# Performance work log

Measured on AMD Instinct MI355X. Metric: run time of the kernel, lower is better.

The kernel has to match this reference:

```python
import jax, jax.numpy as jnp
import numpy as np

B, NQ, NKV, D = 2, 2048, 4096, 1024
H, DH = 16, 64            # qk_channels = v_channels = 1024 -> 16 heads x 64
HID = 2 * int(4.0 * D)    # GEGLU produces 8192 -> split into 2x4096
EPS = 1e-6


def layernorm(x, scale, bias):
    mu = jnp.mean(x, axis=-1, keepdims=True)
    var = jnp.mean(jnp.square(x - mu), axis=-1, keepdims=True)
    return (x - mu) * jax.lax.rsqrt(var + EPS) * scale + bias


def setup_inputs() -> dict:
    key = jax.random.key(0)
    ks = jax.random.split(key, 12)
    s = 0.02
    return {
        "inputs_q": jax.random.normal(ks[0], (B, NQ, D), jnp.float32),
        "inputs_kv": jax.random.normal(ks[1], (B, NKV, D), jnp.float32),
        "ln_q_scale": jnp.ones((D,), jnp.float32),
        "ln_q_bias": jnp.zeros((D,), jnp.float32),
        "ln_kv_scale": jnp.ones((D,), jnp.float32),
        "ln_kv_bias": jnp.zeros((D,), jnp.float32),
        "Wq": s * jax.random.normal(ks[2], (D, H, DH), jnp.float32),
        "bq": jnp.zeros((H, DH), jnp.float32),
        "Wk": s * jax.random.normal(ks[3], (D, H, DH), jnp.float32),
        "bk": jnp.zeros((H, DH), jnp.float32),
        "Wv": s * jax.random.normal(ks[4], (D, H, DH), jnp.float32),
        "bv": jnp.zeros((H, DH), jnp.float32),
        "Wo": s * jax.random.normal(ks[5], (H, DH, D), jnp.float32),
        "bo": jnp.zeros((D,), jnp.float32),
        "ln2_scale": jnp.ones((D,), jnp.float32),
        "ln2_bias": jnp.zeros((D,), jnp.float32),
        "W1": s * jax.random.normal(ks[6], (D, HID), jnp.float32),
        "b1": jnp.zeros((HID,), jnp.float32),
        "W2": s * jax.random.normal(ks[7], (HID // 2, D), jnp.float32),
        "b2": jnp.zeros((D,), jnp.float32),
    }


def reference(inputs_q, inputs_kv, ln_q_scale, ln_q_bias, ln_kv_scale, ln_kv_bias,
              Wq, bq, Wk, bk, Wv, bv, Wo, bo, ln2_scale, ln2_bias, W1, b1, W2, b2):
    ln_q = layernorm(inputs_q, ln_q_scale, ln_q_bias)
    ln_kv = layernorm(inputs_kv, ln_kv_scale, ln_kv_bias)
    # multi-head projections: DenseGeneral to (H, DH)
    q = jnp.einsum('bqd,dhe->bqhe', ln_q, Wq) + bq
    k = jnp.einsum('bkd,dhe->bkhe', ln_kv, Wk) + bk
    v = jnp.einsum('bkd,dhe->bkhe', ln_kv, Wv) + bv
    # scaled dot-product attention (full score matrix, as in source)
    attn = jnp.einsum('bqhd,bkhd->bhqk', q, k) / np.sqrt(DH).astype(np.float32)
    attn = jax.nn.softmax(attn, axis=-1)
    o = jnp.einsum('bhqk,bkhd->bqhd', attn, v)
    # output projection contracting (H, DH)
    x = jnp.einsum('bqhd,hdo->bqo', o, Wo) + bo
    x = x + inputs_q  # query residual
    # GEGLU MLP
    h = layernorm(x, ln2_scale, ln2_bias)
    h = jnp.dot(h, W1) + b1
    a, g = jnp.split(h, 2, axis=-1)
    h = a * jax.nn.gelu(g)  # approximate (tanh) gelu, flax default
    y = jnp.dot(h, W2) + b2
    return x + y
```

## Files before the change

### kernel.cpp

```cpp
#include <hip/hip_runtime.h>

typedef unsigned short u16;
typedef unsigned int u32;
typedef float f32x4 __attribute__((ext_vector_type(4)));
typedef float f32x16 __attribute__((ext_vector_type(16)));
typedef __bf16 bf16x8 __attribute__((ext_vector_type(8)));
typedef short s16x8 __attribute__((ext_vector_type(8)));
typedef short s16x4 __attribute__((ext_vector_type(4)));
typedef u32 u32x4 __attribute__((ext_vector_type(4)));

#define MFMA16(a, b, c) __builtin_amdgcn_mfma_f32_16x16x32_bf16((a), (b), (c), 0, 0, 0)
#define MFMA32(a, b, c) __builtin_amdgcn_mfma_f32_32x32x16_bf16((a), (b), (c), 0, 0, 0)

typedef const __attribute__((address_space(1))) void* gas1_t;
typedef __attribute__((address_space(3))) void* las3_t;
#define GLDS16(g, l) __builtin_amdgcn_global_load_lds((gas1_t)(g), (las3_t)(l), 16, 0, 0)

static __device__ __forceinline__ u16 f2bf(float f) {
  u32 u = __builtin_bit_cast(u32, f);
  u += 0x7FFFu + ((u >> 16) & 1u);
  return (u16)(u >> 16);
}
static __device__ __forceinline__ float bf2f(u16 h) {
  return __builtin_bit_cast(float, (u32)h << 16);
}
static __device__ __forceinline__ u32 cvtpk(float lo, float hi) {
  u32 r;
  asm("v_cvt_pk_bf16_f32 %0, %1, %2" : "=v"(r) : "v"(lo), "v"(hi));
  return r;
}
static __device__ __forceinline__ float gelu_t(float g) {
  float u = 0.7978845608f * (g + 0.044715f * g * g * g);
  float e = __expf(2.0f * u);
  float t = 1.0f - 2.0f / (e + 1.0f);
  return 0.5f * g * (1.0f + t);
}

__global__ __launch_bounds__(256) void transp_cvt(const float* __restrict__ in,
                                                  u16* __restrict__ out, int K, int N,
                                                  float scale) {
  __shared__ u16 t[64][72];
  int k0 = blockIdx.x * 64, n0 = blockIdx.y * 64;
#pragma unroll
  for (int i = 0; i < 16; ++i) {
    int idx = threadIdx.x + i * 256;
    int r = idx >> 6, c = idx & 63;
    t[r][c] = f2bf(in[(size_t)(k0 + r) * N + n0 + c] * scale);
  }
  __syncthreads();
#pragma unroll
  for (int i = 0; i < 16; ++i) {
    int idx = threadIdx.x + i * 256;
    int r = idx >> 6, c = idx & 63;
    out[(size_t)(n0 + r) * K + k0 + c] = t[c][r];
  }
}

__global__ __launch_bounds__(256) void geglu_transp(const float* __restrict__ in,
                                                    u16* __restrict__ out) {
  __shared__ u16 t[64][72];
  int k0 = blockIdx.x * 64, n0 = blockIdx.y * 64;
#pragma unroll
  for (int i = 0; i < 16; ++i) {
    int idx = threadIdx.x + i * 256;
    int r = idx >> 6, c = idx & 63;
    int np = n0 + c;
    int orig = ((np >> 5) << 4) + (np & 15) + (((np >> 4) & 1) << 12);
    t[r][c] = f2bf(in[(size_t)(k0 + r) * 8192 + orig]);
  }
  __syncthreads();
#pragma unroll
  for (int i = 0; i < 16; ++i) {
    int idx = threadIdx.x + i * 256;
    int r = idx >> 6, c = idx & 63;
    out[(size_t)(n0 + r) * 1024 + k0 + c] = t[c][r];
  }
}

__global__ __launch_bounds__(256) void ln_bf16(const float* __restrict__ x,
                                               const float* __restrict__ sc,
                                               const float* __restrict__ bi,
                                               u16* __restrict__ out) {
  int row = blockIdx.x;
  int tid = threadIdx.x;
  float4 v = ((const float4*)(x + (size_t)row * 1024))[tid];
  float s = v.x + v.y + v.z + v.w;
  float s2 = v.x * v.x + v.y * v.y + v.z * v.z + v.w * v.w;
  for (int m = 1; m < 64; m <<= 1) {
    s += __shfl_xor(s, m);
    s2 += __shfl_xor(s2, m);
  }
  __shared__ float rs[4], rs2[4];
  int wave = tid >> 6, lane = tid & 63;
  if (lane == 0) { rs[wave] = s; rs2[wave] = s2; }
  __syncthreads();
  s = rs[0] + rs[1] + rs[2] + rs[3];
  s2 = rs2[0] + rs2[1] + rs2[2] + rs2[3];
  float mu = s * (1.0f / 1024.0f);
  float var = s2 * (1.0f / 1024.0f) - mu * mu;
  float inv = rsqrtf(var + 1e-6f);
  float4 scv = ((const float4*)sc)[tid];
  float4 biv = ((const float4*)bi)[tid];
  s16x4 o;
  o[0] = (short)f2bf((v.x - mu) * inv * scv.x + biv.x);
  o[1] = (short)f2bf((v.y - mu) * inv * scv.y + biv.y);
  o[2] = (short)f2bf((v.z - mu) * inv * scv.z + biv.z);
  o[3] = (short)f2bf((v.w - mu) * inv * scv.w + biv.w);
  *(s16x4*)(out + (size_t)row * 1024 + tid * 4) = o;
}

template <int MODE>
__global__ __launch_bounds__(256) void gemm_nt(const u16* __restrict__ A,
                                               const u16* __restrict__ Bt,
                                               const float* __restrict__ bias,
                                               const float* __restrict__ resid,
                                               void* __restrict__ Cout,
                                               int M, int N, int K, float bias_scale) {
  __shared__ u16 As[128 * 64];
  __shared__ u16 Bs[128 * 64];
  const int nbx = gridDim.x;
  const int nwg = nbx * gridDim.y;
  const int wg0 = blockIdx.y * nbx + blockIdx.x;
  const int wg = (nwg & 7) ? wg0 : (wg0 & 7) * (nwg >> 3) + (wg0 >> 3);
  const int m0 = (wg % nbx) * 128, n0 = (wg / nbx) * 128;
  const int tid = threadIdx.x;
  const int lane = tid & 63, wave = tid >> 6;
  const int wm = (wave >> 1) * 64, wn = (wave & 1) * 64;
  const int lr = lane & 15, hi4 = lane >> 4;
  f32x4 acc[4][4] = {};
  for (int k0 = 0; k0 < K; k0 += 64) {
#pragma unroll
    for (int i = 0; i < 4; ++i) {
      int s = i * 256 + tid;
      int r = s >> 3, slot = s & 7;
      int gslot = slot ^ (r & 7);
      int ldst = (i * 256 + wave * 64) * 8;
      GLDS16(A + (size_t)(m0 + r) * K + k0 + gslot * 8, &As[ldst]);
      GLDS16(Bt + (size_t)(n0 + r) * K + k0 + gslot * 8, &Bs[ldst]);
    }
    __syncthreads();
#pragma unroll
    for (int ks = 0; ks < 2; ++ks) {
      const int sl = ((ks * 4 + hi4) ^ (lr & 7)) * 8;
      bf16x8 af[4], bfr[4];
#pragma unroll
      for (int t = 0; t < 4; ++t) {
        af[t] = __builtin_bit_cast(bf16x8, *(const s16x8*)&As[(wm + t * 16 + lr) * 64 + sl]);
        bfr[t] = __builtin_bit_cast(bf16x8, *(const s16x8*)&Bs[(wn + t * 16 + lr) * 64 + sl]);
      }
#pragma unroll
      for (int mt = 0; mt < 4; ++mt)
#pragma unroll
        for (int nt = 0; nt < 4; ++nt)
          acc[mt][nt] = MFMA16(af[mt], bfr[nt], acc[mt][nt]);
    }
    __syncthreads();
  }
  if constexpr (MODE == 3) {
#pragma unroll
    for (int mt = 0; mt < 4; ++mt) {
      const int mbase = m0 + wm + mt * 16 + hi4 * 4;
#pragma unroll
      for (int p = 0; p < 2; ++p) {
        const int oc = (((n0 + wn + p * 32) >> 5) << 4) + lr;
        const float ba = bias[oc];
        const float bg = bias[oc + 4096];
#pragma unroll
        for (int r = 0; r < 4; ++r) {
          const int m = mbase + r;
          float a = acc[mt][2 * p][r] + ba;
          float g = acc[mt][2 * p + 1][r] + bg;
          ((u16*)Cout)[(size_t)m * 4096 + oc] = f2bf(a * gelu_t(g));
        }
      }
    }
  } else {
#pragma unroll
    for (int mt = 0; mt < 4; ++mt) {
#pragma unroll
      for (int nt = 0; nt < 4; ++nt) {
        const int ncol = n0 + wn + nt * 16 + lr;
        const float bv = bias[ncol] * bias_scale;
        const int mbase = m0 + wm + mt * 16 + hi4 * 4;
#pragma unroll
        for (int r = 0; r < 4; ++r) {
          const int m = mbase + r;
          const float val = acc[mt][nt][r] + bv;
          if constexpr (MODE == 0) {
            ((u16*)Cout)[(size_t)m * N + ncol] = f2bf(val);
          } else if constexpr (MODE == 1) {
            size_t vidx = ((size_t)((m >> 12) * 1024 + ncol) << 12) | (size_t)(m & 4095);
            ((u16*)Cout)[vidx] = f2bf(val);
          } else {
            ((float*)Cout)[(size_t)m * N + ncol] = val + resid[(size_t)m * N + ncol];
          }
        }
      }
    }
  }
}

__global__ __launch_bounds__(256, 2) void flash_attn(const u16* __restrict__ Qg,
                                                     const u16* __restrict__ Kg,
                                                     const u16* __restrict__ Vt,
                                                     u16* __restrict__ Og) {
  __shared__ u16 Ks[2][64 * 64];
  __shared__ u16 Vs[2][64 * 64];
  const int id = blockIdx.x;
  const int bh = (id & 7) * 4 + ((id >> 3) & 3);
  const int qb = id >> 5;
  const int b = bh >> 4, h = bh & 15;
  const int q0 = qb * 128;
  const int tid = threadIdx.x;
  const int lane = tid & 63, wave = tid >> 6;
  const int lq = lane & 31, hi = lane >> 5;
  const u16* Kbase = Kg + (size_t)(b * 4096) * 1024 + h * 64;
  const u16* Vbase = Vt + (size_t)((b * 16 + h) * 64) * 4096;
  bf16x8 qf[4];
  const size_t qrow = (size_t)(b * 2048 + q0 + wave * 32 + lq);
#pragma unroll
  for (int dc = 0; dc < 4; ++dc)
    qf[dc] = __builtin_bit_cast(bf16x8, *(const s16x8*)&Qg[qrow * 1024 + h * 64 + dc * 16 + hi * 8]);

  f32x16 oacc0 = {}, oacc1 = {};
  float lrun = 0.0f;

  auto stage = [&](int buf, int tile) {
    const int kv0 = tile * 64;
#pragma unroll
    for (int i = 0; i < 2; ++i) {
      int s = i * 256 + tid;
      int r = s >> 3;
      int inb = ((s & 7) * 16) ^ ((r & 7) << 4);
      GLDS16(Kbase + (size_t)(kv0 + r) * 1024 + (inb >> 1), &Ks[buf][(i * 256 + wave * 64) * 8]);
    }
#pragma unroll
    for (int i = 0; i < 2; ++i) {
      int s = i * 256 + tid;
      int r = s >> 3;
      int inb = ((s & 7) * 16) ^ ((r & 7) << 4);
      GLDS16(Vbase + (size_t)r * 4096 + kv0 + (inb >> 1), &Vs[buf][(i * 256 + wave * 64) * 8]);
    }
  };

  stage(0, 0);
  __syncthreads();
  int cur = 0;
  for (int t = 0; t < 64; ++t) {
    if (t < 63) stage(cur ^ 1, t + 1);
    f32x16 sA = {}, sB = {};
    __builtin_amdgcn_s_setprio(1);
#pragma unroll
    for (int dc = 0; dc < 4; ++dc) {
      int row = lq;
      int inb = (dc * 32 + hi * 16) ^ ((row & 7) << 4);
      bf16x8 kf = __builtin_bit_cast(bf16x8, *(const s16x8*)&Ks[cur][row * 64 + (inb >> 1)]);
      sA = MFMA32(kf, qf[dc], sA);
    }
#pragma unroll
    for (int dc = 0; dc < 4; ++dc) {
      int row = 32 + lq;
      int inb = (dc * 32 + hi * 16) ^ ((row & 7) << 4);
      bf16x8 kf = __builtin_bit_cast(bf16x8, *(const s16x8*)&Ks[cur][row * 64 + (inb >> 1)]);
      sB = MFMA32(kf, qf[dc], sB);
    }
    __builtin_amdgcn_s_setprio(0);
#pragma unroll
    for (int i = 0; i < 16; ++i) sA[i] = __builtin_amdgcn_exp2f(sA[i]);
#pragma unroll
    for (int i = 0; i < 16; ++i) sB[i] = __builtin_amdgcn_exp2f(sB[i]);
    float a0 = (sA[0] + sA[1]) + (sA[2] + sA[3]);
    float a1 = (sA[4] + sA[5]) + (sA[6] + sA[7]);
    float a2 = (sA[8] + sA[9]) + (sA[10] + sA[11]);
    float a3 = (sA[12] + sA[13]) + (sA[14] + sA[15]);
    float b0 = (sB[0] + sB[1]) + (sB[2] + sB[3]);
    float b1s = (sB[4] + sB[5]) + (sB[6] + sB[7]);
    float b2s = (sB[8] + sB[9]) + (sB[10] + sB[11]);
    float b3 = (sB[12] + sB[13]) + (sB[14] + sB[15]);
    float ts = ((a0 + a1) + (a2 + a3)) + ((b0 + b1s) + (b2s + b3));
    ts += __shfl_xor(ts, 32);
    lrun += ts;
    u32 wa[8], wb[8];
#pragma unroll
    for (int i = 0; i < 8; ++i) wa[i] = cvtpk(sA[2 * i], sA[2 * i + 1]);
#pragma unroll
    for (int i = 0; i < 8; ++i) wb[i] = cvtpk(sB[2 * i], sB[2 * i + 1]);
    u32 a0w = wa[0], c0 = wa[2];
    asm("v_permlane32_swap_b32 %0, %1" : "+v"(a0w), "+v"(c0));
    u32 a1w = wa[1], c1 = wa[3];
    asm("v_permlane32_swap_b32 %0, %1" : "+v"(a1w), "+v"(c1));
    u32 a2w = wa[4], c2 = wa[6];
    asm("v_permlane32_swap_b32 %0, %1" : "+v"(a2w), "+v"(c2));
    u32 a3w = wa[5], c3 = wa[7];
    asm("v_permlane32_swap_b32 %0, %1" : "+v"(a3w), "+v"(c3));
    u32 e0 = wb[0], g0 = wb[2];
    asm("v_permlane32_swap_b32 %0, %1" : "+v"(e0), "+v"(g0));
    u32 e1 = wb[1], g1 = wb[3];
    asm("v_permlane32_swap_b32 %0, %1" : "+v"(e1), "+v"(g1));
    u32 e2 = wb[4], g2 = wb[6];
    asm("v_permlane32_swap_b32 %0, %1" : "+v"(e2), "+v"(g2));
    u32 e3 = wb[5], g3 = wb[7];
    asm("v_permlane32_swap_b32 %0, %1" : "+v"(e3), "+v"(g3));
    u32x4 t00 = {a0w, a1w, c0, c1};
    u32x4 t01 = {a2w, a3w, c2, c3};
    u32x4 t10 = {e0, e1, g0, g1};
    u32x4 t11 = {e2, e3, g2, g3};
    bf16x8 p00 = __builtin_bit_cast(bf16x8, t00);
    bf16x8 p01 = __builtin_bit_cast(bf16x8, t01);
    bf16x8 p10 = __builtin_bit_cast(bf16x8, t10);
    bf16x8 p11 = __builtin_bit_cast(bf16x8, t11);
    __builtin_amdgcn_s_setprio(1);
#pragma unroll
    for (int st = 0; st < 2; ++st) {
      bf16x8 pc0 = st ? p10 : p00;
      bf16x8 pc1 = st ? p11 : p01;
#pragma unroll
      for (int c = 0; c < 2; ++c) {
        bf16x8 pf = c ? pc1 : pc0;
        {
          int row = lq;
          int inb = (st * 64 + c * 32 + hi * 16) ^ ((row & 7) << 4);
          bf16x8 vf = __builtin_bit_cast(bf16x8, *(const s16x8*)&Vs[cur][row * 64 + (inb >> 1)]);
          oacc0 = MFMA32(vf, pf, oacc0);
        }
        {
          int row = 32 + lq;
          int inb = (st * 64 + c * 32 + hi * 16) ^ ((row & 7) << 4);
          bf16x8 vf = __builtin_bit_cast(bf16x8, *(const s16x8*)&Vs[cur][row * 64 + (inb >> 1)]);
          oacc1 = MFMA32(vf, pf, oacc1);
        }
      }
    }
    __builtin_amdgcn_s_setprio(0);
    __syncthreads();
    cur ^= 1;
  }
  float rinv = 1.0f / lrun;
  u16* obase = Og + qrow * 1024 + h * 64;
#pragma unroll
  for (int rp = 0; rp < 8; ++rp) {
    int r0 = rp * 2;
    int d0 = (r0 & 3) + 8 * (r0 >> 2) + 4 * hi;
    *(u32*)&obase[d0] = cvtpk(oacc0[r0] * rinv, oacc0[r0 + 1] * rinv);
    *(u32*)&obase[32 + d0] = cvtpk(oacc1[r0] * rinv, oacc1[r0 + 1] * rinv);
  }
}

extern "C" void kernel_launch(void* const* d_in, const int* in_sizes, int n_in,
                              void* d_out, int out_size, void* d_ws, size_t ws_size,
                              hipStream_t stream) {
  (void)in_sizes; (void)n_in; (void)out_size; (void)ws_size;
  const float* inputs_q = (const float*)d_in[0];
  const float* inputs_kv = (const float*)d_in[1];
  const float* ln_q_scale = (const float*)d_in[2];
  const float* ln_q_bias = (const float*)d_in[3];
  const float* ln_kv_scale = (const float*)d_in[4];
  const float* ln_kv_bias = (const float*)d_in[5];
  const float* Wq = (const float*)d_in[6];
  const float* bq = (const float*)d_in[7];
  const float* Wk = (const float*)d_in[8];
  const float* bk = (const float*)d_in[9];
  const float* Wv = (const float*)d_in[10];
  const float* bv = (const float*)d_in[11];
  const float* Wo = (const float*)d_in[12];
  const float* bo = (const float*)d_in[13];
  const float* ln2_scale = (const float*)d_in[14];
  const float* ln2_bias = (const float*)d_in[15];
  const float* W1 = (const float*)d_in[16];
  const float* b1 = (const float*)d_in[17];
  const float* W2 = (const float*)d_in[18];
  const float* b2 = (const float*)d_in[19];
  float* out = (float*)d_out;
  char* ws = (char*)d_ws;
  const size_t MB = 1ull << 20;
  u16* lnq = (u16*)(ws + 0);
  u16* lnkv = (u16*)(ws + 8 * MB);
  u16* Qb = (u16*)(ws + 24 * MB);
  u16* Kb = (u16*)(ws + 32 * MB);
  u16* Vtb = (u16*)(ws + 48 * MB);
  u16* Ob = (u16*)(ws + 64 * MB);
  float* xbuf = (float*)(ws + 72 * MB);
  u16* ln2b = (u16*)(ws + 88 * MB);
  u16* gg = (u16*)(ws + 96 * MB);
  u16* wqt = (u16*)(ws + 128 * MB);
  u16* wkt = (u16*)(ws + 130 * MB);
  u16* wvt = (u16*)(ws + 132 * MB);
  u16* wot = (u16*)(ws + 134 * MB);
  u16* w1i = (u16*)(ws + 136 * MB);
  u16* w2t = (u16*)(ws + 152 * MB);

  const float QSC = 0.125f * 1.44269504088896f;
  dim3 blk(256);
  transp_cvt<<<dim3(16, 16), blk, 0, stream>>>(Wq, wqt, 1024, 1024, QSC);
  transp_cvt<<<dim3(16, 16), blk, 0, stream>>>(Wk, wkt, 1024, 1024, 1.0f);
  transp_cvt<<<dim3(16, 16), blk, 0, stream>>>(Wv, wvt, 1024, 1024, 1.0f);
  transp_cvt<<<dim3(16, 16), blk, 0, stream>>>(Wo, wot, 1024, 1024, 1.0f);
  geglu_transp<<<dim3(16, 128), blk, 0, stream>>>(W1, w1i);
  transp_cvt<<<dim3(64, 16), blk, 0, stream>>>(W2, w2t, 4096, 1024, 1.0f);
  ln_bf16<<<4096, blk, 0, stream>>>(inputs_q, ln_q_scale, ln_q_bias, lnq);
  ln_bf16<<<8192, blk, 0, stream>>>(inputs_kv, ln_kv_scale, ln_kv_bias, lnkv);
  gemm_nt<0><<<dim3(32, 8), blk, 0, stream>>>(lnq, wqt, bq, nullptr, Qb, 4096, 1024, 1024, QSC);
  gemm_nt<0><<<dim3(64, 8), blk, 0, stream>>>(lnkv, wkt, bk, nullptr, Kb, 8192, 1024, 1024, 1.0f);
  gemm_nt<1><<<dim3(64, 8), blk, 0, stream>>>(lnkv, wvt, bv, nullptr, Vtb, 8192, 1024, 1024, 1.0f);
  flash_attn<<<dim3(512), blk, 0, stream>>>(Qb, Kb, Vtb, Ob);
  gemm_nt<2><<<dim3(32, 8), blk, 0, stream>>>(Ob, wot, bo, inputs_q, xbuf, 4096, 1024, 1024, 1.0f);
  ln_bf16<<<4096, blk, 0, stream>>>(xbuf, ln2_scale, ln2_bias, ln2b);
  gemm_nt<3><<<dim3(32, 64), blk, 0, stream>>>(ln2b, w1i, b1, nullptr, gg, 4096, 8192, 1024, 1.0f);
  gemm_nt<2><<<dim3(32, 8), blk, 0, stream>>>(gg, w2t, b2, xbuf, out, 4096, 1024, 4096, 1.0f);
}
```

Measured before the change: 410.5 us.

## Add 256x256 tiled GEMM kernel for fused K/V projection and GEGLU up-projection

Introduces a new 512-thread GEMM kernel with 256x256 output tiles, double-buffered LDS filled by direct global-to-LDS loads, explicit barriers/waitcnts, and MFMA priority hints. K and V projections are merged into one GEMM over a concatenated weight matrix, with the epilogue routing columns to the K buffer or the transposed V buffer. The GEGLU up-projection also moves to this kernel. The aim is more data reuse per tile and fewer launches, at the cost of higher register/LDS pressure and fewer blocks per GEMM.

New measurement: 409.5 us. Within noise of the previous version (-0.3%).

```diff
diff --git a/kernel.cpp b/kernel.cpp
--- a/kernel.cpp
+++ b/kernel.cpp
@@ -156,44 +156,167 @@
     }
     __syncthreads();
   }
-  if constexpr (MODE == 3) {
-#pragma unroll
-    for (int mt = 0; mt < 4; ++mt) {
+#pragma unroll
+  for (int mt = 0; mt < 4; ++mt) {
+#pragma unroll
+    for (int nt = 0; nt < 4; ++nt) {
+      const int ncol = n0 + wn + nt * 16 + lr;
+      const float bv = bias[ncol] * bias_scale;
       const int mbase = m0 + wm + mt * 16 + hi4 * 4;
 #pragma unroll
+      for (int r = 0; r < 4; ++r) {
+        const int m = mbase + r;
+        const float val = acc[mt][nt][r] + bv;
+        if constexpr (MODE == 0) {
+          ((u16*)Cout)[(size_t)m * N + ncol] = f2bf(val);
+        } else {
+          ((float*)Cout)[(size_t)m * N + ncol] = val + resid[(size_t)m * N + ncol];
+        }
+      }
+    }
+  }
+}
+
+template <int MODE>
+__global__ __launch_bounds__(512, 2) void gemm256(const u16* __restrict__ A,
+                                                  const u16* __restrict__ Bt,
+                                                  const float* __restrict__ bias,
+                                                  const float* __restrict__ bias2,
+                                                  u16* __restrict__ Cout,
+                                                  u16* __restrict__ Vout,
+                                                  int M, int N, int K, int nmajor) {
+  __shared__ __align__(16) u16 sA[2][2][256 * 32];
+  __shared__ __align__(16) u16 sB[2][2][256 * 32];
+  const int nbx = M >> 8, nby = N >> 8;
+  const int nblk = nbx * nby;
+  const int cpx = nblk >> 3;
+  const int wg0 = blockIdx.x;
+  const int wg = (wg0 & 7) * cpx + (wg0 >> 3);
+  int mi, ni;
+  if (nmajor) { ni = wg % nby; mi = wg / nby; } else { mi = wg % nbx; ni = wg / nbx; }
+  const int m0 = mi << 8, n0 = ni << 8;
+  const int tid = threadIdx.x;
+  const int lane = tid & 63, wave = tid >> 6;
+  const int wr = wave >> 2, wc = wave & 3;
+  const int lr = lane & 15, hi4 = lane >> 4;
+  const int rdoct = (hi4 ^ ((lr >> 1) & 3)) * 8;
+  const int NT = K >> 6;
+
+  auto stageA = [&](int t, int kh) {
+#pragma unroll
+    for (int i = 0; i < 2; ++i) {
+      int idx = i * 512 + tid;
+      int r = idx >> 2, go = (idx & 3) ^ ((r >> 1) & 3);
+      GLDS16(A + (size_t)(m0 + r) * K + t * 64 + kh * 32 + go * 8,
+             &sA[t & 1][kh][(i * 512 + wave * 64) * 8]);
+    }
+  };
+  auto stageB = [&](int t, int kh) {
+#pragma unroll
+    for (int i = 0; i < 2; ++i) {
+      int idx = i * 512 + tid;
+      int r = idx >> 2, go = (idx & 3) ^ ((r >> 1) & 3);
+      GLDS16(Bt + (size_t)(n0 + r) * K + t * 64 + kh * 32 + go * 8,
+             &sB[t & 1][kh][(i * 512 + wave * 64) * 8]);
+    }
+  };
+
+  f32x4 acc[8][4] = {};
+  bf16x8 af[4], bf[4];
+
+  stageA(0, 0); stageB(0, 0); stageA(0, 1); stageB(0, 1);
+  asm volatile("s_waitcnt vmcnt(4)" ::: "memory");
+  __builtin_amdgcn_s_barrier();
+  __builtin_amdgcn_sched_barrier(0);
+
+  for (int t = 0; t < NT; ++t) {
+    const int buf = t & 1;
+    const bool pre = (t + 1 < NT);
+#pragma unroll
+    for (int kh = 0; kh < 2; ++kh) {
+#pragma unroll
+      for (int nt = 0; nt < 4; ++nt)
+        bf[nt] = __builtin_bit_cast(bf16x8,
+            *(const s16x8*)&sB[buf][kh][(wc * 64 + nt * 16 + lr) * 32 + rdoct]);
+#pragma unroll
+      for (int mf = 0; mf < 4; ++mf)
+        af[mf] = __builtin_bit_cast(bf16x8,
+            *(const s16x8*)&sA[buf][kh][(wr * 128 + mf * 16 + lr) * 32 + rdoct]);
+      if (pre) stageA(t + 1, kh);
+      __builtin_amdgcn_s_barrier();
+      asm volatile("s_waitcnt lgkmcnt(0)" ::: "memory");
+      __builtin_amdgcn_sched_barrier(0);
+      __builtin_amdgcn_s_setprio(1);
+#pragma unroll
+      for (int mf = 0; mf < 4; ++mf)
+#pragma unroll
+        for (int nt = 0; nt < 4; ++nt)
+          acc[mf][nt] = MFMA16(af[mf], bf[nt], acc[mf][nt]);
+      __builtin_amdgcn_s_setprio(0);
+      __builtin_amdgcn_s_barrier();
+      __builtin_amdgcn_sched_barrier(0);
+#pragma unroll
+      for (int mf = 0; mf < 4; ++mf)
+        af[mf] = __builtin_bit_cast(bf16x8,
+            *(const s16x8*)&sA[buf][kh][(wr * 128 + (4 + mf) * 16 + lr) * 32 + rdoct]);
+      if (pre) stageB(t + 1, kh);
+      __builtin_amdgcn_s_barrier();
+      asm volatile("s_waitcnt lgkmcnt(0)" ::: "memory");
+      __builtin_amdgcn_sched_barrier(0);
+      __builtin_amdgcn_s_setprio(1);
+#pragma unroll
+      for (int mf = 0; mf < 4; ++mf)
+#pragma unroll
+        for (int nt = 0; nt < 4; ++nt)
+          acc[4 + mf][nt] = MFMA16(af[mf], bf[nt], acc[4 + mf][nt]);
+      __builtin_amdgcn_s_setprio(0);
+      if (pre)
+        asm volatile("s_waitcnt vmcnt(4)" ::: "memory");
+      else
+        asm volatile("s_waitcnt vmcnt(0)" ::: "memory");
+      __builtin_amdgcn_s_barrier();
+      __builtin_amdgcn_sched_barrier(0);
+    }
+  }
+
+  if constexpr (MODE == 0) {
+#pragma unroll
+    for (int mf = 0; mf < 8; ++mf) {
+#pragma unroll
+      for (int nt = 0; nt < 4; ++nt) {
+        const int ncol = n0 + wc * 64 + nt * 16 + lr;
+        const int mbase = m0 + wr * 128 + mf * 16 + hi4 * 4;
+        const bool isk = ncol < 1024;
+        const int vc = isk ? ncol : ncol - 1024;
+        const float bv = isk ? bias[ncol] : bias2[vc];
+#pragma unroll
+        for (int r = 0; r < 4; ++r) {
+          const int m = mbase + r;
+          const float val = acc[mf][nt][r] + bv;
+          if (isk) {
+            Cout[(size_t)m * 1024 + ncol] = f2bf(val);
+          } else {
+            size_t vidx = ((size_t)((m >> 12) * 1024 + vc) << 12) | (size_t)(m & 4095);
+            Vout[vidx] = f2bf(val);
+          }
+        }
+      }
+    }
+  } else {
+#pragma unroll
+    for (int mf = 0; mf < 8; ++mf) {
+      const int mbase = m0 + wr * 128 + mf * 16 + hi4 * 4;
+#pragma unroll
       for (int p = 0; p < 2; ++p) {
-        const int oc = (((n0 + wn + p * 32) >> 5) << 4) + lr;
+        const int oc = (((n0 + wc * 64 + p * 32) >> 5) << 4) + lr;
         const float ba = bias[oc];
         const float bg = bias[oc + 4096];
 #pragma unroll
         for (int r = 0; r < 4; ++r) {
           const int m = mbase + r;
-          float a = acc[mt][2 * p][r] + ba;
-          float g = acc[mt][2 * p + 1][r] + bg;
-          ((u16*)Cout)[(size_t)m * 4096 + oc] = f2bf(a * gelu_t(g));
-        }
-      }
-    }
-  } else {
-#pragma unroll
-    for (int mt = 0; mt < 4; ++mt) {
-#pragma unroll
-      for (int nt = 0; nt < 4; ++nt) {
-        const int ncol = n0 + wn + nt * 16 + lr;
-        const float bv = bias[ncol] * bias_scale;
-        const int mbase = m0 + wm + mt * 16 + hi4 * 4;
-#pragma unroll
-        for (int r = 0; r < 4; ++r) {
-          const int m = mbase + r;
-          const float val = acc[mt][nt][r] + bv;
-          if constexpr (MODE == 0) {
-            ((u16*)Cout)[(size_t)m * N + ncol] = f2bf(val);
-          } else if constexpr (MODE == 1) {
-            size_t vidx = ((size_t)((m >> 12) * 1024 + ncol) << 12) | (size_t)(m & 4095);
-            ((u16*)Cout)[vidx] = f2bf(val);
-          } else {
-            ((float*)Cout)[(size_t)m * N + ncol] = val + resid[(size_t)m * N + ncol];
-          }
+          float a = acc[mf][2 * p][r] + ba;
+          float g = acc[mf][2 * p + 1][r] + bg;
+          Cout[(size_t)m * 4096 + oc] = f2bf(a * gelu_t(g));
         }
       }
     }
@@ -383,8 +506,7 @@
   u16* ln2b = (u16*)(ws + 88 * MB);
   u16* gg = (u16*)(ws + 96 * MB);
   u16* wqt = (u16*)(ws + 128 * MB);
-  u16* wkt = (u16*)(ws + 130 * MB);
-  u16* wvt = (u16*)(ws + 132 * MB);
+  u16* wkvt = (u16*)(ws + 130 * MB);
   u16* wot = (u16*)(ws + 134 * MB);
   u16* w1i = (u16*)(ws + 136 * MB);
   u16* w2t = (u16*)(ws + 152 * MB);
@@ -392,19 +514,18 @@
   const float QSC = 0.125f * 1.44269504088896f;
   dim3 blk(256);
   transp_cvt<<<dim3(16, 16), blk, 0, stream>>>(Wq, wqt, 1024, 1024, QSC);
-  transp_cvt<<<dim3(16, 16), blk, 0, stream>>>(Wk, wkt, 1024, 1024, 1.0f);
-  transp_cvt<<<dim3(16, 16), blk, 0, stream>>>(Wv, wvt, 1024, 1024, 1.0f);
+  transp_cvt<<<dim3(16, 16), blk, 0, stream>>>(Wk, wkvt, 1024, 1024, 1.0f);
+  transp_cvt<<<dim3(16, 16), blk, 0, stream>>>(Wv, wkvt + 1024 * 1024, 1024, 1024, 1.0f);
   transp_cvt<<<dim3(16, 16), blk, 0, stream>>>(Wo, wot, 1024, 1024, 1.0f);
   geglu_transp<<<dim3(16, 128), blk, 0, stream>>>(W1, w1i);
   transp_cvt<<<dim3(64, 16), blk, 0, stream>>>(W2, w2t, 4096, 1024, 1.0f);
   ln_bf16<<<4096, blk, 0, stream>>>(inputs_q, ln_q_scale, ln_q_bias, lnq);
   ln_bf16<<<8192, blk, 0, stream>>>(inputs_kv, ln_kv_scale, ln_kv_bias, lnkv);
   gemm_nt<0><<<dim3(32, 8), blk, 0, stream>>>(lnq, wqt, bq, nullptr, Qb, 4096, 1024, 1024, QSC);
-  gemm_nt<0><<<dim3(64, 8), blk, 0, stream>>>(lnkv, wkt, bk, nullptr, Kb, 8192, 1024, 1024, 1.0f);
-  gemm_nt<1><<<dim3(64, 8), blk, 0, stream>>>(lnkv, wvt, bv, nullptr, Vtb, 8192, 1024, 1024, 1.0f);
+  gemm256<0><<<dim3(256), dim3(512), 0, stream>>>(lnkv, wkvt, bk, bv, Kb, Vtb, 8192, 2048, 1024, 1);
   flash_attn<<<dim3(512), blk, 0, stream>>>(Qb, Kb, Vtb, Ob);
   gemm_nt<2><<<dim3(32, 8), blk, 0, stream>>>(Ob, wot, bo, inputs_q, xbuf, 4096, 1024, 1024, 1.0f);
   ln_bf16<<<4096, blk, 0, stream>>>(xbuf, ln2_scale, ln2_bias, ln2b);
-  gemm_nt<3><<<dim3(32, 64), blk, 0, stream>>>(ln2b, w1i, b1, nullptr, gg, 4096, 8192, 1024, 1.0f);
+  gemm256<1><<<dim3(512), dim3(512), 0, stream>>>(ln2b, w1i, b1, nullptr, gg, nullptr, 4096, 8192, 1024, 0);
   gemm_nt<2><<<dim3(32, 8), blk, 0, stream>>>(gg, w2t, b2, xbuf, out, 4096, 1024, 4096, 1.0f);
 }
```
